# Kernel tuning notes

Hardware: AMD Instinct MI355X
Metric: run time of the kernel (lower is better)

The kernel has to match this reference:

```python
import jax, jax.numpy as jnp
import numpy as np

B, S, F, P, D, H, L, FF, R = 64, 4096, 8, 16, 512, 8, 6, 2048, 8
NP = (S - P) // P + 1  # 256 patches (stride == patch_length)
DK = D // H
LORA_SCALING = 16.0 / 8.0  # lora_alpha / lora_rank


def setup_inputs() -> dict:
    key = jax.random.key(0)
    ks = iter(jax.random.split(key, 40))
    def nrm(shape, s=0.02):
        return jax.random.normal(next(ks), shape, jnp.float32) * s
    inp = {
        "x": jax.random.normal(next(ks), (B, S, F), jnp.float32),
        "patch_w": nrm((P * F, D)), "patch_b": jnp.zeros((D,), jnp.float32),
        "patch_ln_w": jnp.ones((D,), jnp.float32), "patch_ln_b": jnp.zeros((D,), jnp.float32),
        "pos_enc": nrm((1, NP, D)),
        "ln1_w": jnp.ones((L, D), jnp.float32), "ln1_b": jnp.zeros((L, D), jnp.float32),
        "q_w": nrm((L, D, D)), "q_b": jnp.zeros((L, D), jnp.float32),
        "k_w": nrm((L, D, D)), "k_b": jnp.zeros((L, D), jnp.float32),
        "v_w": nrm((L, D, D)), "v_b": jnp.zeros((L, D), jnp.float32),
        "lq_down": nrm((L, D, R)), "lq_up": nrm((L, R, D)),
        "lk_down": nrm((L, D, R)), "lk_up": nrm((L, R, D)),
        "lv_down": nrm((L, D, R)), "lv_up": nrm((L, R, D)),
        "o_w": nrm((L, D, D)), "o_b": jnp.zeros((L, D), jnp.float32),
        "ln2_w": jnp.ones((L, D), jnp.float32), "ln2_b": jnp.zeros((L, D), jnp.float32),
        "ff1_w": nrm((L, D, FF)), "ff1_b": jnp.zeros((L, FF), jnp.float32),
        "ff2_w": nrm((L, FF, D)), "ff2_b": jnp.zeros((L, D), jnp.float32),
        "norm_w": jnp.ones((D,), jnp.float32), "norm_b": jnp.zeros((D,), jnp.float32),
    }
    return inp


def _layer_norm(x, w, b):
    m = jnp.mean(x, -1, keepdims=True)
    v = jnp.mean(jnp.square(x - m), -1, keepdims=True)
    return (x - m) * jax.lax.rsqrt(v + 1e-5) * w + b


def _forward(x, patch_w, patch_b, patch_ln_w, patch_ln_b, pos_enc,
             ln1_w, ln1_b, q_w, q_b, k_w, k_b, v_w, v_b,
             lq_down, lq_up, lk_down, lk_up, lv_down, lv_up,
             o_w, o_b, ln2_w, ln2_b, ff1_w, ff1_b, ff2_w, ff2_b,
             norm_w, norm_b):
    # Patch embedding: [B,S,F] -> [B,F,S] -> unfold(stride==patch) -> [B,NP,F*P]
    patches = x.transpose(0, 2, 1).reshape(B, F, NP, P).transpose(0, 2, 1, 3).reshape(B, NP, F * P)
    h = _layer_norm(patches @ patch_w + patch_b, patch_ln_w, patch_ln_b) + pos_enc
    inv_scale = 1.0 / np.sqrt(DK).astype(np.float32)
    for i in range(L):
        y = _layer_norm(h, ln1_w[i], ln1_b[i])
        q = y @ q_w[i] + q_b[i] + (y @ lq_down[i]) @ lq_up[i] * LORA_SCALING
        k = y @ k_w[i] + k_b[i] + (y @ lk_down[i]) @ lk_up[i] * LORA_SCALING
        v = y @ v_w[i] + v_b[i] + (y @ lv_down[i]) @ lv_up[i] * LORA_SCALING
        q = q.reshape(B, NP, H, DK)
        k = k.reshape(B, NP, H, DK)
        v = v.reshape(B, NP, H, DK)
        scores = jnp.einsum('bqhd,bkhd->bhqk', q, k) * inv_scale
        probs = jax.nn.softmax(scores, axis=-1)
        attn = jnp.einsum('bhqk,bkhd->bqhd', probs, v).reshape(B, NP, D)
        h = h + attn @ o_w[i] + o_b[i]
        y = _layer_norm(h, ln2_w[i], ln2_b[i])
        ff = jax.nn.gelu(y @ ff1_w[i] + ff1_b[i], approximate=False) @ ff2_w[i] + ff2_b[i]
        h = h + ff
    h = _layer_norm(h, norm_w, norm_b)
    return h.mean(axis=1)  # [B, D]


def reference(x, patch_w, patch_b, patch_ln_w, patch_ln_b, pos_enc,
              ln1_w, ln1_b, q_w, q_b, k_w, k_b, v_w, v_b,
              lq_down, lq_up, lk_down, lk_up, lv_down, lv_up,
              o_w, o_b, ln2_w, ln2_b, ff1_w, ff1_b, ff2_w, ff2_b,
              norm_w, norm_b):
    return _forward(x, patch_w, patch_b, patch_ln_w, patch_ln_b, pos_enc,
                    ln1_w, ln1_b, q_w, q_b, k_w, k_b, v_w, v_b,
                    lq_down, lq_up, lk_down, lk_up, lv_down, lv_up,
                    o_w, o_b, ln2_w, ln2_b, ff1_w, ff1_b, ff2_w, ff2_b,
                    norm_w, norm_b)
```

## Files before the change

### kernel.cpp

```cpp
#include <hip/hip_runtime.h>
#include <cstdint>
#include <cstddef>

constexpr int BATCH = 64, SEQ = 4096, FEAT = 8, PLEN = 16;
constexpr int DMODEL = 512, NHEAD = 8, NLAYER = 6, DFF = 2048;
constexpr int NPATCH = 256, MROWS = BATCH * NPATCH;
constexpr int DK = 64;
constexpr int LDSP = 72;

typedef unsigned short u16t;
typedef __bf16 bf16t;
typedef bf16t bf16x8 __attribute__((ext_vector_type(8)));
typedef short s16x4 __attribute__((ext_vector_type(4)));
typedef float f32x4 __attribute__((ext_vector_type(4)));

__device__ __forceinline__ float b2f(u16t u) {
  union { unsigned int ui; float f; } v; v.ui = ((unsigned int)u) << 16; return v.f;
}
__device__ __forceinline__ u16t f2b(float f) {
  union { float f; unsigned int ui; } v; v.f = f;
  return (u16t)((v.ui + 0x7fffu + ((v.ui >> 16) & 1u)) >> 16);
}
__device__ __forceinline__ void g2l16(void* lds, const void* g) {
  __builtin_amdgcn_global_load_lds(
      (__attribute__((address_space(1))) void*)g,
      (__attribute__((address_space(3))) void*)lds, 16, 0, 0);
}

__device__ __forceinline__ float gelu_erf(float x) {
  const float z = fabsf(x) * 0.70710678118654752f;
  const float t = __builtin_amdgcn_rcpf(__builtin_fmaf(0.3275911f, z, 1.0f));
  float p = __builtin_fmaf(1.061405429f, t, -1.453152027f);
  p = __builtin_fmaf(p, t, 1.421413741f);
  p = __builtin_fmaf(p, t, -0.284496736f);
  p = __builtin_fmaf(p, t, 0.254829592f);
  const float e = __expf(-z * z);
  const float er = __builtin_fmaf(-p * t, e, 1.0f);
  const float s = copysignf(er, x);
  return 0.5f * x * (1.0f + s);
}

__global__ __launch_bounds__(256) void k_gemm(
    const u16t* __restrict__ A, const u16t* __restrict__ Bt,
    const float* __restrict__ bias, const float* __restrict__ b2,
    const float* __restrict__ b3, float* __restrict__ Cf,
    u16t* __restrict__ Cb, int M, int N, int K, int mode)
{
  __shared__ __align__(16) u16t SH[2 * 128 * 64];
  u16t* As = SH;
  u16t* Bs = SH + 128 * 64;
  const int bm = blockIdx.x * 128, bn = blockIdx.y * 128;
  const int tid = threadIdx.x, wave = tid >> 6, lane = tid & 63;
  const int wm = (wave & 1) << 6, wn = (wave >> 1) << 6;
  const int lr = lane & 15, quad = lane >> 4;
  const int srow = lane >> 3;
  const int scol = (((lane & 7) ^ srow) * 8);

  f32x4 acc[4][4] = {};
  const u16t* Ab = A + (size_t)bm * K;
  const u16t* Bb = Bt + (size_t)bn * K;

  for (int k0 = 0; k0 < K; k0 += 64) {
    #pragma unroll
    for (int j = 0; j < 4; ++j) {
      const int r0 = (wave * 4 + j) * 8;
      g2l16(&As[r0 * 64], Ab + (size_t)(r0 + srow) * K + k0 + scol);
      g2l16(&Bs[r0 * 64], Bb + (size_t)(r0 + srow) * K + k0 + scol);
    }
    __syncthreads();
    #pragma unroll
    for (int ks = 0; ks < 64; ks += 32) {
      bf16x8 af[4], bfr[4];
      const int segb = ks >> 3;
      #pragma unroll
      for (int i = 0; i < 4; ++i)
        af[i] = *(const bf16x8*)&As[(wm + i * 16 + lr) * 64 + (((segb + quad) ^ (lr & 7)) * 8)];
      #pragma unroll
      for (int j = 0; j < 4; ++j)
        bfr[j] = *(const bf16x8*)&Bs[(wn + j * 16 + lr) * 64 + (((segb + quad) ^ (lr & 7)) * 8)];
      #pragma unroll
      for (int j = 0; j < 4; ++j)
        #pragma unroll
        for (int i = 0; i < 4; ++i)
          acc[j][i] = __builtin_amdgcn_mfma_f32_16x16x32_bf16(bfr[j], af[i], acc[j][i], 0, 0, 0);
    }
    __syncthreads();
  }

  const float* bp = bias;
  int reg0 = 0;
  if (bias && b2) { reg0 = (bn >> 9) << 9; bp = reg0 == 0 ? bias : (reg0 == 512 ? b2 : b3); }
  float4 bv[4];
  #pragma unroll
  for (int jN = 0; jN < 4; ++jN) {
    const int gn0 = bn + wn + jN * 16 + quad * 4;
    bv[jN] = bias ? *(const float4*)&bp[gn0 - reg0] : make_float4(0.f, 0.f, 0.f, 0.f);
  }

  if (mode <= 1) {
    u16t* E = SH;
    #pragma unroll
    for (int jN = 0; jN < 4; ++jN) {
      const int cl = wn + jN * 16 + quad * 4;
      const int seg = cl >> 3, intra = cl & 7;
      #pragma unroll
      for (int iM = 0; iM < 4; ++iM) {
        const int r = wm + iM * 16 + lr;
        float v0 = acc[jN][iM][0] + bv[jN].x, v1 = acc[jN][iM][1] + bv[jN].y;
        float v2 = acc[jN][iM][2] + bv[jN].z, v3 = acc[jN][iM][3] + bv[jN].w;
        union { u16t h[4]; uint2 u; } pk;
        if (mode == 1) {
          pk.h[0] = f2b(gelu_erf(v0)); pk.h[1] = f2b(gelu_erf(v1));
          pk.h[2] = f2b(gelu_erf(v2)); pk.h[3] = f2b(gelu_erf(v3));
        } else {
          pk.h[0] = f2b(v0); pk.h[1] = f2b(v1); pk.h[2] = f2b(v2); pk.h[3] = f2b(v3);
        }
        *(uint2*)&E[r * 128 + ((seg ^ (r & 7)) << 3) + intra] = pk.u;
      }
    }
    __syncthreads();
    const int rr = tid >> 2, s0 = tid & 3;
    #pragma unroll
    for (int pass = 0; pass < 2; ++pass) {
      const int r = pass * 64 + rr;
      u16t* gout = Cb + (size_t)(bm + r) * N + bn;
      #pragma unroll
      for (int it = 0; it < 4; ++it) {
        const int s = s0 + it * 4;
        uint4 u = *(const uint4*)&E[r * 128 + ((s ^ (r & 7)) << 3)];
        *(uint4*)(gout + s * 8) = u;
      }
    }
  } else {
    #pragma unroll
    for (int jN = 0; jN < 4; ++jN) {
      const int gn0 = bn + wn + jN * 16 + quad * 4;
      #pragma unroll
      for (int iM = 0; iM < 4; ++iM) {
        const int gm = bm + wm + iM * 16 + lr;
        const size_t off = (size_t)gm * N + gn0;
        float v0 = acc[jN][iM][0] + bv[jN].x, v1 = acc[jN][iM][1] + bv[jN].y;
        float v2 = acc[jN][iM][2] + bv[jN].z, v3 = acc[jN][iM][3] + bv[jN].w;
        if (mode == 2) {
          float4 c = *(float4*)(Cf + off);
          c.x += v0; c.y += v1; c.z += v2; c.w += v3;
          *(float4*)(Cf + off) = c;
        } else {
          *(float4*)(Cf + off) = make_float4(v0, v1, v2, v3);
        }
      }
    }
  }
}

__global__ __launch_bounds__(256) void k_prep_w(
    const float* __restrict__ W, const float* __restrict__ down,
    const float* __restrict__ up, u16t* __restrict__ Wt, int K, int N,
    size_t ostride, int orow0)
{
  __shared__ float t[32][33];
  const int z = blockIdx.z;
  const float* Wz = W + (size_t)z * K * N;
  u16t* Wtz = Wt + (size_t)z * ostride + (size_t)orow0 * K;
  const int k0 = blockIdx.x * 32, n0 = blockIdx.y * 32;
  const int tx = threadIdx.x & 31, ty = threadIdx.x >> 5;
  for (int i = ty; i < 32; i += 8) {
    const int kk = k0 + i, nn = n0 + tx;
    float v = Wz[(size_t)kk * N + nn];
    if (down) {
      const float* dz = down + (size_t)z * K * 8 + (size_t)kk * 8;
      const float* uz = up + (size_t)z * 8 * N + nn;
      float lv = 0.f;
      #pragma unroll
      for (int r = 0; r < 8; ++r) lv += dz[r] * uz[(size_t)r * N];
      v += 2.0f * lv;
    }
    t[i][tx] = v;
  }
  __syncthreads();
  for (int i = ty; i < 32; i += 8)
    Wtz[(size_t)(n0 + i) * K + k0 + tx] = f2b(t[tx][i]);
}

__global__ void k_patch(const float* __restrict__ x, u16t* __restrict__ pt) {
  const int idx = blockIdx.x * 256 + threadIdx.x;
  const int col = idx & 127, row = idx >> 7;
  const int f = col >> 4, pp = col & 15;
  const int b = row >> 8, np = row & 255;
  pt[idx] = f2b(x[(((size_t)b << 12) + np * 16 + pp) * 8 + f]);
}

__global__ __launch_bounds__(256) void k_ln(
    const float* __restrict__ xin, const float* __restrict__ w,
    const float* __restrict__ bb, u16t* __restrict__ y)
{
  const int row = blockIdx.x * 4 + (threadIdx.x >> 6);
  const int lane = threadIdx.x & 63;
  const float4* xr = (const float4*)(xin + (size_t)row * 512);
  float4 a = xr[lane * 2], c = xr[lane * 2 + 1];
  float s = a.x + a.y + a.z + a.w + c.x + c.y + c.z + c.w;
  float qq = a.x * a.x + a.y * a.y + a.z * a.z + a.w * a.w +
             c.x * c.x + c.y * c.y + c.z * c.z + c.w * c.w;
  #pragma unroll
  for (int o = 32; o > 0; o >>= 1) { s += __shfl_xor(s, o); qq += __shfl_xor(qq, o); }
  const float mean = s * (1.f / 512.f);
  const float rs = rsqrtf(qq * (1.f / 512.f) - mean * mean + 1e-5f);
  const float4* wr = (const float4*)w; const float4* br = (const float4*)bb;
  float4 w0 = wr[lane * 2], w1 = wr[lane * 2 + 1];
  float4 b0 = br[lane * 2], b1 = br[lane * 2 + 1];
  union { u16t h[8]; uint4 v; } pk;
  pk.h[0] = f2b((a.x - mean) * rs * w0.x + b0.x);
  pk.h[1] = f2b((a.y - mean) * rs * w0.y + b0.y);
  pk.h[2] = f2b((a.z - mean) * rs * w0.z + b0.z);
  pk.h[3] = f2b((a.w - mean) * rs * w0.w + b0.w);
  pk.h[4] = f2b((c.x - mean) * rs * w1.x + b1.x);
  pk.h[5] = f2b((c.y - mean) * rs * w1.y + b1.y);
  pk.h[6] = f2b((c.z - mean) * rs * w1.z + b1.z);
  pk.h[7] = f2b((c.w - mean) * rs * w1.w + b1.w);
  *(uint4*)(y + (size_t)row * 512 + lane * 8) = pk.v;
}

__global__ __launch_bounds__(256) void k_ln_pos(
    const float* __restrict__ xin, const float* __restrict__ w,
    const float* __restrict__ bb, const float* __restrict__ pos,
    float* __restrict__ h)
{
  const int row = blockIdx.x * 4 + (threadIdx.x >> 6);
  const int lane = threadIdx.x & 63;
  const float4* xr = (const float4*)(xin + (size_t)row * 512);
  float4 a = xr[lane * 2], c = xr[lane * 2 + 1];
  float s = a.x + a.y + a.z + a.w + c.x + c.y + c.z + c.w;
  float qq = a.x * a.x + a.y * a.y + a.z * a.z + a.w * a.w +
             c.x * c.x + c.y * c.y + c.z * c.z + c.w * c.w;
  #pragma unroll
  for (int o = 32; o > 0; o >>= 1) { s += __shfl_xor(s, o); qq += __shfl_xor(qq, o); }
  const float mean = s * (1.f / 512.f);
  const float rs = rsqrtf(qq * (1.f / 512.f) - mean * mean + 1e-5f);
  const float4* wr = (const float4*)w; const float4* br = (const float4*)bb;
  float4 w0 = wr[lane * 2], w1 = wr[lane * 2 + 1];
  float4 b0 = br[lane * 2], b1 = br[lane * 2 + 1];
  const int np = row & 255;
  const float4* pr = (const float4*)(pos + (size_t)np * 512);
  float4 p0 = pr[lane * 2], p1 = pr[lane * 2 + 1];
  float4 o0, o1;
  o0.x = (a.x - mean) * rs * w0.x + b0.x + p0.x;
  o0.y = (a.y - mean) * rs * w0.y + b0.y + p0.y;
  o0.z = (a.z - mean) * rs * w0.z + b0.z + p0.z;
  o0.w = (a.w - mean) * rs * w0.w + b0.w + p0.w;
  o1.x = (c.x - mean) * rs * w1.x + b1.x + p1.x;
  o1.y = (c.y - mean) * rs * w1.y + b1.y + p1.y;
  o1.z = (c.z - mean) * rs * w1.z + b1.z + p1.z;
  o1.w = (c.w - mean) * rs * w1.w + b1.w + p1.w;
  float4* hr = (float4*)(h + (size_t)row * 512);
  hr[lane * 2] = o0; hr[lane * 2 + 1] = o1;
}

__global__ __launch_bounds__(256) void k_attn(
    const u16t* __restrict__ qkv, u16t* __restrict__ out)
{
  __shared__ __align__(16) u16t Qs[128 * LDSP];
  __shared__ __align__(16) u16t Ks[64 * LDSP];
  __shared__ __align__(16) u16t Vts[64 * LDSP];

  const int bh = blockIdx.x >> 1, half = blockIdx.x & 1;
  const int b = bh >> 3, hd = bh & 7;
  const int tid = threadIdx.x, wave = tid >> 6, lane = tid & 63;
  const int lr = lane & 15, quad = lane >> 4;

  const size_t rowbase = (size_t)b * 256;
  const u16t* qg = qkv + (rowbase + half * 128) * 1536 + hd * 64;
  const u16t* kg = qkv + rowbase * 1536 + 512 + hd * 64;
  const u16t* vg = qkv + rowbase * 1536 + 1024 + hd * 64;

  #pragma unroll
  for (int i = 0; i < 4; ++i) {
    const int idx = tid + i * 256, row = idx >> 3, seg = idx & 7;
    uint4 u = *(const uint4*)(qg + (size_t)row * 1536 + seg * 8);
    *(uint4*)&Qs[row * LDSP + seg * 8] = u;
  }
  __syncthreads();

  bf16x8 qf[2][2];
  #pragma unroll
  for (int qi = 0; qi < 2; ++qi)
    #pragma unroll
    for (int dh = 0; dh < 2; ++dh)
      qf[qi][dh] = *(const bf16x8*)&Qs[(wave * 32 + qi * 16 + lr) * LDSP + dh * 32 + quad * 8];

  f32x4 O[2][4] = {};
  float mrun[2] = {-1e30f, -1e30f}, lrun[2] = {0.f, 0.f};

  for (int c = 0; c < 4; ++c) {
    __syncthreads();
    #pragma unroll
    for (int i = 0; i < 2; ++i) {
      const int idx = tid + i * 256, row = idx >> 3, seg = idx & 7;
      uint4 u = *(const uint4*)(kg + (size_t)(c * 64 + row) * 1536 + seg * 8);
      *(uint4*)&Ks[row * LDSP + seg * 8] = u;
    }
    {
      const int key = tid & 63, dg = (tid >> 6) * 16;
      const u16t* vrow = vg + (size_t)(c * 64 + key) * 1536 + dg;
      union { u16t h[16]; uint4 v[2]; } tmp;
      tmp.v[0] = *(const uint4*)(vrow);
      tmp.v[1] = *(const uint4*)(vrow + 8);
      #pragma unroll
      for (int i = 0; i < 16; ++i)
        Vts[(dg + i) * LDSP + key] = tmp.h[i];
    }
    __syncthreads();

    #pragma unroll
    for (int qi = 0; qi < 2; ++qi) {
      f32x4 s[4];
      #pragma unroll
      for (int kt = 0; kt < 4; ++kt) {
        f32x4 a = {};
        #pragma unroll
        for (int dh = 0; dh < 2; ++dh) {
          bf16x8 kf = *(const bf16x8*)&Ks[(kt * 16 + lr) * LDSP + dh * 32 + quad * 8];
          a = __builtin_amdgcn_mfma_f32_16x16x32_bf16(kf, qf[qi][dh], a, 0, 0, 0);
        }
        s[kt] = a;
      }
      constexpr float SC = 0.125f * 1.44269504088896f;
      float cmax = -1e30f;
      #pragma unroll
      for (int kt = 0; kt < 4; ++kt)
        #pragma unroll
        for (int r = 0; r < 4; ++r) { s[kt][r] *= SC; cmax = fmaxf(cmax, s[kt][r]); }
      cmax = fmaxf(cmax, __shfl_xor(cmax, 16));
      cmax = fmaxf(cmax, __shfl_xor(cmax, 32));
      const float mn = fmaxf(mrun[qi], cmax);
      const float alpha = exp2f(mrun[qi] - mn);
      mrun[qi] = mn;
      float lsum = 0.f;
      s16x4 pf[4];
      #pragma unroll
      for (int kt = 0; kt < 4; ++kt) {
        #pragma unroll
        for (int r = 0; r < 4; ++r) {
          const u16t eb = f2b(exp2f(s[kt][r] - mn));
          pf[kt][r] = (short)eb;
          lsum += b2f(eb);
        }
      }
      lsum += __shfl_xor(lsum, 16);
      lsum += __shfl_xor(lsum, 32);
      lrun[qi] = lrun[qi] * alpha + lsum;
      #pragma unroll
      for (int dt = 0; dt < 4; ++dt) {
        f32x4 o = O[qi][dt];
        o[0] *= alpha; o[1] *= alpha; o[2] *= alpha; o[3] *= alpha;
        #pragma unroll
        for (int kt = 0; kt < 4; ++kt) {
          s16x4 vf = *(const s16x4*)&Vts[(dt * 16 + lr) * LDSP + kt * 16 + quad * 4];
          o = __builtin_amdgcn_mfma_f32_16x16x16bf16_1k(vf, pf[kt], o, 0, 0, 0);
        }
        O[qi][dt] = o;
      }
    }
  }
  #pragma unroll
  for (int qi = 0; qi < 2; ++qi) {
    const float rl = 1.f / lrun[qi];
    u16t* orow = out + (rowbase + half * 128 + wave * 32 + qi * 16 + lr) * 512 + hd * 64 + quad * 4;
    #pragma unroll
    for (int dt = 0; dt < 4; ++dt) {
      union { u16t h[4]; uint2 v; } pk;
      #pragma unroll
      for (int r = 0; r < 4; ++r) pk.h[r] = f2b(O[qi][dt][r] * rl);
      *(uint2*)(orow + dt * 16) = pk.v;
    }
  }
}

__global__ void k_mean(const u16t* __restrict__ y, float* __restrict__ out) {
  const int b = blockIdx.x, d = threadIdx.x;
  float s = 0.f;
  #pragma unroll 8
  for (int np = 0; np < 256; ++np) s += b2f(y[((size_t)b * 256 + np) * 512 + d]);
  out[(size_t)b * 512 + d] = s * (1.f / 256.f);
}

extern "C" void kernel_launch(void* const* d_in, const int* in_sizes, int n_in,
                              void* d_out, int out_size, void* d_ws, size_t ws_size,
                              hipStream_t stream)
{
  (void)in_sizes; (void)n_in; (void)out_size;
  const float* x        = (const float*)d_in[0];
  const float* patch_w  = (const float*)d_in[1];
  const float* patch_b  = (const float*)d_in[2];
  const float* patch_ln_w = (const float*)d_in[3];
  const float* patch_ln_b = (const float*)d_in[4];
  const float* pos_enc  = (const float*)d_in[5];
  const float* ln1_w    = (const float*)d_in[6];
  const float* ln1_b    = (const float*)d_in[7];
  const float* q_w      = (const float*)d_in[8];
  const float* q_b      = (const float*)d_in[9];
  const float* k_w      = (const float*)d_in[10];
  const float* k_b      = (const float*)d_in[11];
  const float* v_w      = (const float*)d_in[12];
  const float* v_b      = (const float*)d_in[13];
  const float* lq_down  = (const float*)d_in[14];
  const float* lq_up    = (const float*)d_in[15];
  const float* lk_down  = (const float*)d_in[16];
  const float* lk_up    = (const float*)d_in[17];
  const float* lv_down  = (const float*)d_in[18];
  const float* lv_up    = (const float*)d_in[19];
  const float* o_w      = (const float*)d_in[20];
  const float* o_b      = (const float*)d_in[21];
  const float* ln2_w    = (const float*)d_in[22];
  const float* ln2_b    = (const float*)d_in[23];
  const float* ff1_w    = (const float*)d_in[24];
  const float* ff1_b    = (const float*)d_in[25];
  const float* ff2_w    = (const float*)d_in[26];
  const float* ff2_b    = (const float*)d_in[27];
  const float* norm_w   = (const float*)d_in[28];
  const float* norm_b   = (const float*)d_in[29];
  float* out = (float*)d_out;

  char* p = (char*)d_ws;
  float* h  = (float*)p;  p += (size_t)MROWS * 512 * 4;
  u16t*  y  = (u16t*)p;   p += (size_t)MROWS * 512 * 2;
  char* uni = p;          p += (size_t)4 * MROWS * 512 * 2;
  u16t* qkvb = (u16t*)uni;
  u16t* ab = (u16t*)(uni + (size_t)MROWS * 1536 * 2);
  u16t* g  = (u16t*)uni;
  float* pe = (float*)uni;
  u16t* pt = (u16t*)(uni + (size_t)MROWS * 512 * 4);
  u16t* wqkv = (u16t*)p; p += (size_t)NLAYER * 1536 * 512 * 2;
  u16t* wo = (u16t*)p; p += (size_t)NLAYER * 512 * 512 * 2;
  u16t* w1 = (u16t*)p; p += (size_t)NLAYER * 512 * 2048 * 2;
  u16t* w2 = (u16t*)p; p += (size_t)NLAYER * 2048 * 512 * 2;
  u16t* wp = (u16t*)p; p += (size_t)512 * 128 * 2;
  if ((size_t)(p - (char*)d_ws) > ws_size) return;

  const dim3 blk(256);
  const size_t QKVS = (size_t)1536 * 512;
  k_prep_w<<<dim3(16, 16, NLAYER), blk, 0, stream>>>(q_w, lq_down, lq_up, wqkv, 512, 512, QKVS, 0);
  k_prep_w<<<dim3(16, 16, NLAYER), blk, 0, stream>>>(k_w, lk_down, lk_up, wqkv, 512, 512, QKVS, 512);
  k_prep_w<<<dim3(16, 16, NLAYER), blk, 0, stream>>>(v_w, lv_down, lv_up, wqkv, 512, 512, QKVS, 1024);
  k_prep_w<<<dim3(16, 16, NLAYER), blk, 0, stream>>>(o_w, nullptr, nullptr, wo, 512, 512, (size_t)512 * 512, 0);
  k_prep_w<<<dim3(16, 64, NLAYER), blk, 0, stream>>>(ff1_w, nullptr, nullptr, w1, 512, 2048, (size_t)512 * 2048, 0);
  k_prep_w<<<dim3(64, 16, NLAYER), blk, 0, stream>>>(ff2_w, nullptr, nullptr, w2, 2048, 512, (size_t)2048 * 512, 0);
  k_prep_w<<<dim3(4, 16, 1),       blk, 0, stream>>>(patch_w, nullptr, nullptr, wp, 128, 512, 0, 0);

  k_patch<<<dim3(MROWS * 128 / 256), blk, 0, stream>>>(x, pt);
  k_gemm<<<dim3(128, 4), blk, 0, stream>>>(pt, wp, patch_b, nullptr, nullptr, pe, nullptr, MROWS, 512, 128, 3);
  k_ln_pos<<<dim3(MROWS / 4), blk, 0, stream>>>(pe, patch_ln_w, patch_ln_b, pos_enc, h);

  for (int i = 0; i < NLAYER; ++i) {
    const size_t ws512 = (size_t)i * 512 * 512, wsff = (size_t)i * 512 * 2048;
    k_ln<<<dim3(MROWS / 4), blk, 0, stream>>>(h, ln1_w + i * 512, ln1_b + i * 512, y);
    k_gemm<<<dim3(128, 12), blk, 0, stream>>>(y, wqkv + i * QKVS, q_b + i * 512, k_b + i * 512,
                                              v_b + i * 512, nullptr, qkvb, MROWS, 1536, 512, 0);
    k_attn<<<dim3(1024), blk, 0, stream>>>(qkvb, ab);
    k_gemm<<<dim3(128, 4), blk, 0, stream>>>(ab, wo + ws512, o_b + i * 512, nullptr, nullptr, h, nullptr, MROWS, 512, 512, 2);
    k_ln<<<dim3(MROWS / 4), blk, 0, stream>>>(h, ln2_w + i * 512, ln2_b + i * 512, y);
    k_gemm<<<dim3(128, 16), blk, 0, stream>>>(y, w1 + wsff, ff1_b + i * 2048, nullptr, nullptr, nullptr, g, MROWS, 2048, 512, 1);
    k_gemm<<<dim3(128, 4), blk, 0, stream>>>(g, w2 + wsff, ff2_b + i * 512, nullptr, nullptr, h, nullptr, MROWS, 512, 2048, 2);
  }
  k_ln<<<dim3(MROWS / 4), blk, 0, stream>>>(h, norm_w, norm_b, y);
  k_mean<<<dim3(BATCH), dim3(512), 0, stream>>>(y, out);
}
```

Before: 1.603 ms.

## Rewrite GEMM with 256x128 tiles, triple-buffered async loads, and XCD-aware block mapping

```diff
diff --git a/kernel.cpp b/kernel.cpp
--- a/kernel.cpp
+++ b/kernel.cpp
@@ -40,51 +40,94 @@
   return 0.5f * x * (1.0f + s);
 }
 
-__global__ __launch_bounds__(256) void k_gemm(
+__global__ __launch_bounds__(256, 2) void k_gemm(
     const u16t* __restrict__ A, const u16t* __restrict__ Bt,
     const float* __restrict__ bias, const float* __restrict__ b2,
     const float* __restrict__ b3, float* __restrict__ Cf,
     u16t* __restrict__ Cb, int M, int N, int K, int mode)
 {
-  __shared__ __align__(16) u16t SH[2 * 128 * 64];
-  u16t* As = SH;
-  u16t* Bs = SH + 128 * 64;
-  const int bm = blockIdx.x * 128, bn = blockIdx.y * 128;
+  __shared__ __align__(16) u16t SH[3 * 12288];
+
+  const int nbn = N >> 7;
+  const int cpx = gridDim.x >> 3;
+  const int wgid = (blockIdx.x & 7) * cpx + (blockIdx.x >> 3);
+  const int bm = (wgid / nbn) << 8;
+  const int bn = (wgid % nbn) << 7;
+
   const int tid = threadIdx.x, wave = tid >> 6, lane = tid & 63;
-  const int wm = (wave & 1) << 6, wn = (wave >> 1) << 6;
   const int lr = lane & 15, quad = lane >> 4;
-  const int srow = lane >> 3;
-  const int scol = (((lane & 7) ^ srow) * 8);
-
-  f32x4 acc[4][4] = {};
-  const u16t* Ab = A + (size_t)bm * K;
-  const u16t* Bb = Bt + (size_t)bn * K;
-
-  for (int k0 = 0; k0 < K; k0 += 64) {
-    #pragma unroll
-    for (int j = 0; j < 4; ++j) {
-      const int r0 = (wave * 4 + j) * 8;
-      g2l16(&As[r0 * 64], Ab + (size_t)(r0 + srow) * K + k0 + scol);
-      g2l16(&Bs[r0 * 64], Bb + (size_t)(r0 + srow) * K + k0 + scol);
-    }
-    __syncthreads();
-    #pragma unroll
-    for (int ks = 0; ks < 64; ks += 32) {
-      bf16x8 af[4], bfr[4];
-      const int segb = ks >> 3;
-      #pragma unroll
-      for (int i = 0; i < 4; ++i)
-        af[i] = *(const bf16x8*)&As[(wm + i * 16 + lr) * 64 + (((segb + quad) ^ (lr & 7)) * 8)];
-      #pragma unroll
-      for (int j = 0; j < 4; ++j)
-        bfr[j] = *(const bf16x8*)&Bs[(wn + j * 16 + lr) * 64 + (((segb + quad) ^ (lr & 7)) * 8)];
-      #pragma unroll
-      for (int j = 0; j < 4; ++j)
-        #pragma unroll
-        for (int i = 0; i < 4; ++i)
-          acc[j][i] = __builtin_amdgcn_mfma_f32_16x16x32_bf16(bfr[j], af[i], acc[j][i], 0, 0, 0);
-    }
-    __syncthreads();
+  const int wm = (wave >> 1) << 7;
+  const int wn = (wave & 1) << 6;
+
+  const int srow = lane >> 2;
+  const int sseg = (lane & 3) ^ ((lane >> 3) & 3);
+  const u16t* gA = A + (size_t)(bm + wave * 64 + srow) * K + sseg * 8;
+  const u16t* gB = Bt + (size_t)(bn + wave * 32 + srow) * K + sseg * 8;
+  const size_t r16K = (size_t)16 * K;
+
+  const int sw8 = (quad ^ ((lr >> 1) & 3)) << 3;
+  const int aoff = (wm + lr) * 32 + sw8;
+  const int boff = 8192 + (wn + lr) * 32 + sw8;
+
+  f32x4 acc[4][8] = {};
+
+  u16t* buf0 = SH;
+  u16t* buf1 = SH + 12288;
+  u16t* buf2 = SH + 24576;
+
+  #pragma unroll
+  for (int j = 0; j < 4; ++j) g2l16(&buf0[(wave * 4 + j) * 512], gA + (size_t)j * r16K);
+  #pragma unroll
+  for (int j = 0; j < 2; ++j) g2l16(&buf0[8192 + (wave * 2 + j) * 512], gB + (size_t)j * r16K);
+  gA += 32; gB += 32;
+  #pragma unroll
+  for (int j = 0; j < 4; ++j) g2l16(&buf1[(wave * 4 + j) * 512], gA + (size_t)j * r16K);
+  #pragma unroll
+  for (int j = 0; j < 2; ++j) g2l16(&buf1[8192 + (wave * 2 + j) * 512], gB + (size_t)j * r16K);
+  gA += 32; gB += 32;
+
+  const int nt = K >> 5;
+  for (int t = 0; t < nt - 1; ++t) {
+    asm volatile("s_waitcnt vmcnt(6)" ::: "memory");
+    __builtin_amdgcn_s_barrier();
+    asm volatile("" ::: "memory");
+    if (t + 2 < nt) {
+      #pragma unroll
+      for (int j = 0; j < 4; ++j) g2l16(&buf2[(wave * 4 + j) * 512], gA + (size_t)j * r16K);
+      #pragma unroll
+      for (int j = 0; j < 2; ++j) g2l16(&buf2[8192 + (wave * 2 + j) * 512], gB + (size_t)j * r16K);
+      gA += 32; gB += 32;
+    }
+    bf16x8 af[8], bfr[4];
+    #pragma unroll
+    for (int i = 0; i < 8; ++i) af[i] = *(const bf16x8*)&buf0[aoff + i * 512];
+    #pragma unroll
+    for (int j = 0; j < 4; ++j) bfr[j] = *(const bf16x8*)&buf0[boff + j * 512];
+    __builtin_amdgcn_s_setprio(1);
+    #pragma unroll
+    for (int j = 0; j < 4; ++j)
+      #pragma unroll
+      for (int i = 0; i < 8; ++i)
+        acc[j][i] = __builtin_amdgcn_mfma_f32_16x16x32_bf16(bfr[j], af[i], acc[j][i], 0, 0, 0);
+    __builtin_amdgcn_s_setprio(0);
+    u16t* tmp = buf0; buf0 = buf1; buf1 = buf2; buf2 = tmp;
+  }
+  {
+    asm volatile("s_waitcnt vmcnt(0)" ::: "memory");
+    __builtin_amdgcn_s_barrier();
+    asm volatile("" ::: "memory");
+    bf16x8 af[8], bfr[4];
+    #pragma unroll
+    for (int i = 0; i < 8; ++i) af[i] = *(const bf16x8*)&buf0[aoff + i * 512];
+    #pragma unroll
+    for (int j = 0; j < 4; ++j) bfr[j] = *(const bf16x8*)&buf0[boff + j * 512];
+    __builtin_amdgcn_s_setprio(1);
+    #pragma unroll
+    for (int j = 0; j < 4; ++j)
+      #pragma unroll
+      for (int i = 0; i < 8; ++i)
+        acc[j][i] = __builtin_amdgcn_mfma_f32_16x16x32_bf16(bfr[j], af[i], acc[j][i], 0, 0, 0);
+    __builtin_amdgcn_s_setprio(0);
   }
 
   const float* bp = bias;
@@ -98,13 +141,14 @@
   }
 
   if (mode <= 1) {
+    __syncthreads();
     u16t* E = SH;
     #pragma unroll
     for (int jN = 0; jN < 4; ++jN) {
       const int cl = wn + jN * 16 + quad * 4;
       const int seg = cl >> 3, intra = cl & 7;
       #pragma unroll
-      for (int iM = 0; iM < 4; ++iM) {
+      for (int iM = 0; iM < 8; ++iM) {
         const int r = wm + iM * 16 + lr;
         float v0 = acc[jN][iM][0] + bv[jN].x, v1 = acc[jN][iM][1] + bv[jN].y;
         float v2 = acc[jN][iM][2] + bv[jN].z, v3 = acc[jN][iM][3] + bv[jN].w;
@@ -121,7 +165,7 @@
     __syncthreads();
     const int rr = tid >> 2, s0 = tid & 3;
     #pragma unroll
-    for (int pass = 0; pass < 2; ++pass) {
+    for (int pass = 0; pass < 4; ++pass) {
       const int r = pass * 64 + rr;
       u16t* gout = Cb + (size_t)(bm + r) * N + bn;
       #pragma unroll
@@ -136,7 +180,7 @@
     for (int jN = 0; jN < 4; ++jN) {
       const int gn0 = bn + wn + jN * 16 + quad * 4;
       #pragma unroll
-      for (int iM = 0; iM < 4; ++iM) {
+      for (int iM = 0; iM < 8; ++iM) {
         const int gm = bm + wm + iM * 16 + lr;
         const size_t off = (size_t)gm * N + gn0;
         float v0 = acc[jN][iM][0] + bv[jN].x, v1 = acc[jN][iM][1] + bv[jN].y;
@@ -447,19 +491,19 @@
   k_prep_w<<<dim3(4, 16, 1),       blk, 0, stream>>>(patch_w, nullptr, nullptr, wp, 128, 512, 0, 0);
 
   k_patch<<<dim3(MROWS * 128 / 256), blk, 0, stream>>>(x, pt);
-  k_gemm<<<dim3(128, 4), blk, 0, stream>>>(pt, wp, patch_b, nullptr, nullptr, pe, nullptr, MROWS, 512, 128, 3);
+  k_gemm<<<dim3(64 * 4), blk, 0, stream>>>(pt, wp, patch_b, nullptr, nullptr, pe, nullptr, MROWS, 512, 128, 3);
   k_ln_pos<<<dim3(MROWS / 4), blk, 0, stream>>>(pe, patch_ln_w, patch_ln_b, pos_enc, h);
 
   for (int i = 0; i < NLAYER; ++i) {
     const size_t ws512 = (size_t)i * 512 * 512, wsff = (size_t)i * 512 * 2048;
     k_ln<<<dim3(MROWS / 4), blk, 0, stream>>>(h, ln1_w + i * 512, ln1_b + i * 512, y);
-    k_gemm<<<dim3(128, 12), blk, 0, stream>>>(y, wqkv + i * QKVS, q_b + i * 512, k_b + i * 512,
+    k_gemm<<<dim3(64 * 12), blk, 0, stream>>>(y, wqkv + i * QKVS, q_b + i * 512, k_b + i * 512,
                                               v_b + i * 512, nullptr, qkvb, MROWS, 1536, 512, 0);
     k_attn<<<dim3(1024), blk, 0, stream>>>(qkvb, ab);
-    k_gemm<<<dim3(128, 4), blk, 0, stream>>>(ab, wo + ws512, o_b + i * 512, nullptr, nullptr, h, nullptr, MROWS, 512, 512, 2);
+    k_gemm<<<dim3(64 * 4), blk, 0, stream>>>(ab, wo + ws512, o_b + i * 512, nullptr, nullptr, h, nullptr, MROWS, 512, 512, 2);
     k_ln<<<dim3(MROWS / 4), blk, 0, stream>>>(h, ln2_w + i * 512, ln2_b + i * 512, y);
-    k_gemm<<<dim3(128, 16), blk, 0, stream>>>(y, w1 + wsff, ff1_b + i * 2048, nullptr, nullptr, nullptr, g, MROWS, 2048, 512, 1);
-    k_gemm<<<dim3(128, 4), blk, 0, stream>>>(g, w2 + wsff, ff2_b + i * 512, nullptr, nullptr, h, nullptr, MROWS, 512, 2048, 2);
+    k_gemm<<<dim3(64 * 16), blk, 0, stream>>>(y, w1 + wsff, ff1_b + i * 2048, nullptr, nullptr, nullptr, g, MROWS, 2048, 512, 1);
+    k_gemm<<<dim3(64 * 4), blk, 0, stream>>>(g, w2 + wsff, ff2_b + i * 512, nullptr, nullptr, h, nullptr, MROWS, 512, 2048, 2);
   }
   k_ln<<<dim3(MROWS / 4), blk, 0, stream>>>(h, norm_w, norm_b, y);
   k_mean<<<dim3(BATCH), dim3(512), 0, stream>>>(y, out);
```

Result: faster. 1.501 ms (-6.4%).

## Rewrite GEMM as 256x128 tile, 4-stage LDS pipeline with XCD-aware block mapping

Applied to the files above, without the earlier changes.

```diff
diff --git a/kernel.cpp b/kernel.cpp
--- a/kernel.cpp
+++ b/kernel.cpp
@@ -40,52 +40,79 @@
   return 0.5f * x * (1.0f + s);
 }
 
-__global__ __launch_bounds__(256) void k_gemm(
+__global__ __launch_bounds__(512, 2) void k_gemm(
     const u16t* __restrict__ A, const u16t* __restrict__ Bt,
     const float* __restrict__ bias, const float* __restrict__ b2,
     const float* __restrict__ b3, float* __restrict__ Cf,
     u16t* __restrict__ Cb, int M, int N, int K, int mode)
 {
-  __shared__ __align__(16) u16t SH[2 * 128 * 64];
-  u16t* As = SH;
-  u16t* Bs = SH + 128 * 64;
-  const int bm = blockIdx.x * 128, bn = blockIdx.y * 128;
+  __shared__ __align__(16) u16t SH[4 * 12288];
+
+  const int nbn = N >> 7;
+  const int cpx = gridDim.x >> 3;
+  const int wgid = (blockIdx.x & 7) * cpx + (blockIdx.x >> 3);
+  const int bm = (wgid / nbn) << 8;
+  const int bn = (wgid % nbn) << 7;
+
   const int tid = threadIdx.x, wave = tid >> 6, lane = tid & 63;
-  const int wm = (wave & 1) << 6, wn = (wave >> 1) << 6;
   const int lr = lane & 15, quad = lane >> 4;
-  const int srow = lane >> 3;
-  const int scol = (((lane & 7) ^ srow) * 8);
+  const int wm = (wave >> 1) << 6;
+  const int wn = (wave & 1) << 6;
+
+  const int sseg = (lane & 3) ^ ((lane >> 3) & 3);
+  const u16t* gA0 = A + (size_t)(bm + (lane >> 2)) * K + sseg * 8;
+  const u16t* gB0 = Bt + (size_t)(bn + (lane >> 2)) * K + sseg * 8;
+
+  const int sw8 = (quad ^ ((lr >> 1) & 3)) << 3;
+  const int aoff = (wm + lr) * 32 + sw8;
+  const int boff = 8192 + (wn + lr) * 32 + sw8;
 
   f32x4 acc[4][4] = {};
-  const u16t* Ab = A + (size_t)bm * K;
-  const u16t* Bb = Bt + (size_t)bn * K;
-
-  for (int k0 = 0; k0 < K; k0 += 64) {
-    #pragma unroll
-    for (int j = 0; j < 4; ++j) {
-      const int r0 = (wave * 4 + j) * 8;
-      g2l16(&As[r0 * 64], Ab + (size_t)(r0 + srow) * K + k0 + scol);
-      g2l16(&Bs[r0 * 64], Bb + (size_t)(r0 + srow) * K + k0 + scol);
-    }
-    __syncthreads();
-    #pragma unroll
-    for (int ks = 0; ks < 64; ks += 32) {
-      bf16x8 af[4], bfr[4];
-      const int segb = ks >> 3;
-      #pragma unroll
-      for (int i = 0; i < 4; ++i)
-        af[i] = *(const bf16x8*)&As[(wm + i * 16 + lr) * 64 + (((segb + quad) ^ (lr & 7)) * 8)];
-      #pragma unroll
-      for (int j = 0; j < 4; ++j)
-        bfr[j] = *(const bf16x8*)&Bs[(wn + j * 16 + lr) * 64 + (((segb + quad) ^ (lr & 7)) * 8)];
-      #pragma unroll
-      for (int j = 0; j < 4; ++j)
-        #pragma unroll
-        for (int i = 0; i < 4; ++i)
-          acc[j][i] = __builtin_amdgcn_mfma_f32_16x16x32_bf16(bfr[j], af[i], acc[j][i], 0, 0, 0);
-    }
-    __syncthreads();
-  }
+
+  const int nt = K >> 5;
+
+#define STAGE3(S_) do {                                                        \
+    u16t* dA_ = SH + (((S_) & 3) * 12288);                                     \
+    g2l16(dA_ + wave * 512,       gA0 + (size_t)(wave * 16) * K + (S_) * 32);  \
+    g2l16(dA_ + (wave + 8) * 512, gA0 + (size_t)((wave + 8) * 16) * K + (S_) * 32); \
+    g2l16(dA_ + 8192 + wave * 512, gB0 + (size_t)(wave * 16) * K + (S_) * 32); \
+  } while (0)
+
+#define NPHASE(S_, NG_) do {                                                   \
+    const int s_ = (S_);                                                       \
+    const int slot_ = (s_ & 3) * 12288;                                        \
+    bf16x8 af_[4], bfr_[4];                                                    \
+    _Pragma("unroll")                                                          \
+    for (int i = 0; i < 4; ++i)                                                \
+      af_[i] = *(const bf16x8*)&SH[slot_ + aoff + i * 512];                    \
+    _Pragma("unroll")                                                          \
+    for (int j = 0; j < 4; ++j)                                                \
+      bfr_[j] = *(const bf16x8*)&SH[slot_ + boff + j * 512];                   \
+    if (s_ + 3 < nt) STAGE3(s_ + 3);                                           \
+    __builtin_amdgcn_s_barrier();                                              \
+    asm volatile("s_waitcnt lgkmcnt(0)" ::: "memory");                         \
+    __builtin_amdgcn_sched_barrier(0);                                         \
+    __builtin_amdgcn_s_setprio(1);                                             \
+    _Pragma("unroll")                                                          \
+    for (int j = 0; j < 4; ++j)                                                \
+      _Pragma("unroll")                                                        \
+      for (int i = 0; i < 4; ++i)                                              \
+        acc[j][i] = __builtin_amdgcn_mfma_f32_16x16x32_bf16(bfr_[j], af_[i], acc[j][i], 0, 0, 0); \
+    __builtin_amdgcn_s_setprio(0);                                             \
+    asm volatile("s_waitcnt vmcnt(" #NG_ ")" ::: "memory");                    \
+    __builtin_amdgcn_s_barrier();                                              \
+  } while (0)
+
+  STAGE3(0); STAGE3(1); STAGE3(2);
+  asm volatile("s_waitcnt vmcnt(6)" ::: "memory");
+  __builtin_amdgcn_s_barrier();
+
+  for (int s = 0; s < nt - 3; ++s) NPHASE(s, 6);
+  NPHASE(nt - 3, 3);
+  NPHASE(nt - 2, 0);
+  NPHASE(nt - 1, 0);
+#undef NPHASE
+#undef STAGE3
 
   const float* bp = bias;
   int reg0 = 0;
@@ -98,6 +125,7 @@
   }
 
   if (mode <= 1) {
+    __syncthreads();
     u16t* E = SH;
     #pragma unroll
     for (int jN = 0; jN < 4; ++jN) {
@@ -122,7 +150,7 @@
     const int rr = tid >> 2, s0 = tid & 3;
     #pragma unroll
     for (int pass = 0; pass < 2; ++pass) {
-      const int r = pass * 64 + rr;
+      const int r = pass * 128 + rr;
       u16t* gout = Cb + (size_t)(bm + r) * N + bn;
       #pragma unroll
       for (int it = 0; it < 4; ++it) {
@@ -437,6 +465,7 @@
   if ((size_t)(p - (char*)d_ws) > ws_size) return;
 
   const dim3 blk(256);
+  const dim3 gblk(512);
   const size_t QKVS = (size_t)1536 * 512;
   k_prep_w<<<dim3(16, 16, NLAYER), blk, 0, stream>>>(q_w, lq_down, lq_up, wqkv, 512, 512, QKVS, 0);
   k_prep_w<<<dim3(16, 16, NLAYER), blk, 0, stream>>>(k_w, lk_down, lk_up, wqkv, 512, 512, QKVS, 512);
@@ -447,19 +476,19 @@
   k_prep_w<<<dim3(4, 16, 1),       blk, 0, stream>>>(patch_w, nullptr, nullptr, wp, 128, 512, 0, 0);
 
   k_patch<<<dim3(MROWS * 128 / 256), blk, 0, stream>>>(x, pt);
-  k_gemm<<<dim3(128, 4), blk, 0, stream>>>(pt, wp, patch_b, nullptr, nullptr, pe, nullptr, MROWS, 512, 128, 3);
+  k_gemm<<<dim3(64 * 4), gblk, 0, stream>>>(pt, wp, patch_b, nullptr, nullptr, pe, nullptr, MROWS, 512, 128, 3);
   k_ln_pos<<<dim3(MROWS / 4), blk, 0, stream>>>(pe, patch_ln_w, patch_ln_b, pos_enc, h);
 
   for (int i = 0; i < NLAYER; ++i) {
     const size_t ws512 = (size_t)i * 512 * 512, wsff = (size_t)i * 512 * 2048;
     k_ln<<<dim3(MROWS / 4), blk, 0, stream>>>(h, ln1_w + i * 512, ln1_b + i * 512, y);
-    k_gemm<<<dim3(128, 12), blk, 0, stream>>>(y, wqkv + i * QKVS, q_b + i * 512, k_b + i * 512,
-                                              v_b + i * 512, nullptr, qkvb, MROWS, 1536, 512, 0);
+    k_gemm<<<dim3(64 * 12), gblk, 0, stream>>>(y, wqkv + i * QKVS, q_b + i * 512, k_b + i * 512,
+                                               v_b + i * 512, nullptr, qkvb, MROWS, 1536, 512, 0);
     k_attn<<<dim3(1024), blk, 0, stream>>>(qkvb, ab);
-    k_gemm<<<dim3(128, 4), blk, 0, stream>>>(ab, wo + ws512, o_b + i * 512, nullptr, nullptr, h, nullptr, MROWS, 512, 512, 2);
+    k_gemm<<<dim3(64 * 4), gblk, 0, stream>>>(ab, wo + ws512, o_b + i * 512, nullptr, nullptr, h, nullptr, MROWS, 512, 512, 2);
     k_ln<<<dim3(MROWS / 4), blk, 0, stream>>>(h, ln2_w + i * 512, ln2_b + i * 512, y);
-    k_gemm<<<dim3(128, 16), blk, 0, stream>>>(y, w1 + wsff, ff1_b + i * 2048, nullptr, nullptr, nullptr, g, MROWS, 2048, 512, 1);
-    k_gemm<<<dim3(128, 4), blk, 0, stream>>>(g, w2 + wsff, ff2_b + i * 512, nullptr, nullptr, h, nullptr, MROWS, 512, 2048, 2);
+    k_gemm<<<dim3(64 * 16), gblk, 0, stream>>>(y, w1 + wsff, ff1_b + i * 2048, nullptr, nullptr, nullptr, g, MROWS, 2048, 512, 1);
+    k_gemm<<<dim3(64 * 4), gblk, 0, stream>>>(g, w2 + wsff, ff2_b + i * 512, nullptr, nullptr, h, nullptr, MROWS, 512, 2048, 2);
   }
   k_ln<<<dim3(MROWS / 4), blk, 0, stream>>>(h, norm_w, norm_b, y);
   k_mean<<<dim3(BATCH), dim3(512), 0, stream>>>(y, out);
```

New measurement: 1.636 ms. 1.02x slower.
